# Kernel optimization log

Hardware: AMD Instinct MI355X
Metric: run time of the kernel (lower is better)

## Reference

```python
import jax, jax.numpy as jnp
import numpy as np

NUM_CATEGORIES = 32
INPUT_DIM = 1024
HIDDEN_DIM = 4096
BATCH = 64
SEQ = 512


def setup_inputs() -> dict:
    key = jax.random.key(0)
    k_x, k_w, k_c = jax.random.split(key, 3)
    x = jax.random.normal(k_x, (BATCH, SEQ, INPUT_DIM), dtype=jnp.float32)
    W = 0.02 * jax.random.normal(k_w, (NUM_CATEGORIES, INPUT_DIM, HIDDEN_DIM), dtype=jnp.float32)
    b = jnp.zeros((NUM_CATEGORIES, HIDDEN_DIM), dtype=jnp.float32)
    cat_ids = jax.random.randint(k_c, (BATCH,), 0, NUM_CATEGORIES, dtype=jnp.int64)
    return {"x": x, "cat_ids": cat_ids, "W": W, "b": b}


def reference(x, cat_ids, W, b):
    # Gather per-sample weight/bias by category, then batched matmul.
    selected_W = W[cat_ids]              # [B, input_dim, hidden_dim]
    selected_b = b[cat_ids]              # [B, hidden_dim]
    out = jnp.einsum('bsi,bih->bsh', x, selected_W)  # [B, S, hidden_dim]
    return out + selected_b[:, None, :]
```

## Files before the change

kernel.cpp:

```cpp
#include <hip/hip_runtime.h>
#include <stdint.h>

#define B_ 64
#define S_ 512
#define K_ 1024
#define H_ 4096
#define C_ 32

typedef float  f32x4  __attribute__((ext_vector_type(4)));
typedef short  bf16x8 __attribute__((ext_vector_type(8)));
typedef unsigned short u16x8 __attribute__((ext_vector_type(8)));
typedef __attribute__((address_space(3))) unsigned int as3u32;
typedef const __attribute__((address_space(1))) unsigned int as1u32;

__device__ __forceinline__ unsigned short f2bf(float f) {
    unsigned u = __builtin_bit_cast(unsigned, f);
    u += 0x7fffu + ((u >> 16) & 1u);
    return (unsigned short)(u >> 16);
}

__global__ void fix_cat_kernel(const void* __restrict__ cat_raw, int* __restrict__ cat32) {
    int t = threadIdx.x;
    const long long* c64 = (const long long*)cat_raw;
    const int*       c32 = (const int*)cat_raw;
    long long v = (t < 32) ? c64[t] : 0;
    int bad = (t < 32) && (v < 0 || v >= C_);
    unsigned long long m = __ballot(bad);
    if (m == 0ULL) {
        cat32[t] = (int)c64[t];
    } else {
        cat32[t] = c32[t];
    }
}

__global__ __launch_bounds__(256) void cvt_x_kernel(const float4* __restrict__ x,
                                                    uint4* __restrict__ xb, int n8) {
    int stride = gridDim.x * blockDim.x;
    for (int i = blockIdx.x * blockDim.x + threadIdx.x; i < n8; i += stride) {
        float4 a = x[2 * i], b = x[2 * i + 1];
        uint4 o;
        o.x = (unsigned)f2bf(a.x) | ((unsigned)f2bf(a.y) << 16);
        o.y = (unsigned)f2bf(a.z) | ((unsigned)f2bf(a.w) << 16);
        o.z = (unsigned)f2bf(b.x) | ((unsigned)f2bf(b.y) << 16);
        o.w = (unsigned)f2bf(b.z) | ((unsigned)f2bf(b.w) << 16);
        xb[i] = o;
    }
}

__global__ __launch_bounds__(256) void cvt_w_kernel(const float* __restrict__ W,
                                                    unsigned short* __restrict__ WT) {
    __shared__ unsigned short tile[64 * 68];
    const int nt = blockIdx.x;
    const int kt = blockIdx.y;
    const int c  = blockIdx.z;
    const int t  = threadIdx.x;

    const float* Wp = W + ((size_t)c << 22);
#pragma unroll
    for (int p = 0; p < 4; ++p) {
        int task = p * 256 + t;
        int kr = task >> 4;
        int nc = (task & 15) << 2;
        float4 v = *(const float4*)(Wp + (size_t)(kt * 64 + kr) * H_ + nt * 64 + nc);
        tile[kr * 68 + nc + 0] = f2bf(v.x);
        tile[kr * 68 + nc + 1] = f2bf(v.y);
        tile[kr * 68 + nc + 2] = f2bf(v.z);
        tile[kr * 68 + nc + 3] = f2bf(v.w);
    }
    __syncthreads();

    unsigned short* WTp = WT + ((size_t)c << 22);
#pragma unroll
    for (int q = 0; q < 2; ++q) {
        int task = q * 256 + t;
        int nl = task >> 3;
        int ko = (task & 7) << 3;
        u16x8 o;
#pragma unroll
        for (int j = 0; j < 8; ++j) o[j] = tile[(ko + j) * 68 + nl];
        *(u16x8*)(WTp + (size_t)(nt * 64 + nl) * K_ + kt * 64 + ko) = o;
    }
}

__global__ __launch_bounds__(512, 2) void gemm6_kernel(
    const unsigned short* __restrict__ xb,
    const unsigned short* __restrict__ WT,
    const float* __restrict__ bias,
    const int* __restrict__ cat,
    float* __restrict__ out)
{
    extern __shared__ __align__(16) char smem[];

    const int t    = threadIdx.x;
    const int lane = t & 63;
    const int w    = t >> 6;
    const int wm   = w >> 2;
    const int wn   = w & 3;
    const int lo   = lane & 15;
    const int hi   = lane >> 4;

    const int wg = (blockIdx.x & 7) * 256 + (blockIdx.x >> 3);
    const int bn = wg & 15;
    const int bm = (wg >> 4) & 1;
    const int bb = wg >> 5;

    const int c = cat[bb];

    const unsigned short* Ap = xb + (size_t)bb * (S_ * K_) + (size_t)(bm * 256) * K_;
    const unsigned short* Bp = WT + (size_t)c * ((size_t)H_ * K_) + (size_t)(bn * 256) * K_;

    const int srow  = lane >> 2;
    const int sslot = (lane & 3) ^ ((lane >> 3) & 3);
    const char* sA0 = (const char*)(Ap + (size_t)((0 * 8 + w) * 16 + srow) * K_) + sslot * 16;
    const char* sA1 = (const char*)(Ap + (size_t)((1 * 8 + w) * 16 + srow) * K_) + sslot * 16;
    const char* sB0 = (const char*)(Bp + (size_t)((0 * 8 + w) * 16 + srow) * K_) + sslot * 16;
    const char* sB1 = (const char*)(Bp + (size_t)((1 * 8 + w) * 16 + srow) * K_) + sslot * 16;
    const int dc0 = (0 * 8 + w) * 1024;
    const int dc1 = (1 * 8 + w) * 1024;

    const int xslot = (hi ^ ((lo >> 1) & 3)) << 4;
    int aoff[8], boff[4];
#pragma unroll
    for (int mi = 0; mi < 8; ++mi) aoff[mi] = (wm * 128 + mi * 16 + lo) * 64 + xslot;
#pragma unroll
    for (int ni = 0; ni < 4; ++ni) boff[ni] = 16384 + (wn * 64 + ni * 16 + lo) * 64 + xslot;

    f32x4 acc[8][4];
#pragma unroll
    for (int mi = 0; mi < 8; ++mi)
#pragma unroll
        for (int ni = 0; ni < 4; ++ni) acc[mi][ni] = f32x4{0.f, 0.f, 0.f, 0.f};

#define GLD(src_, dst_) __builtin_amdgcn_global_load_lds((as1u32*)(src_), (as3u32*)(dst_), 16, 0, 0)

    {
        char* s0 = smem;
        char* s1 = smem + 32768;
        GLD(sA0 + 0,  s0 + dc0);          GLD(sB0 + 0,  s0 + 16384 + dc0);
        GLD(sA1 + 0,  s0 + dc1);          GLD(sB1 + 0,  s0 + 16384 + dc1);
        GLD(sA0 + 64, s1 + dc0);          GLD(sB0 + 64, s1 + 16384 + dc0);
        GLD(sA1 + 64, s1 + dc1);          GLD(sB1 + 64, s1 + 16384 + dc1);
    }
    asm volatile("s_waitcnt vmcnt(4)" ::: "memory");
    __builtin_amdgcn_s_barrier();

    int rs = 0;
    int ws = 2;

#pragma unroll 1
    for (int T = 0; T < 32; ++T) {
        const char* rb = smem + rs * 32768;
        char*       wb = smem + ws * 32768;
        const int soff = ((T + 2) & 31) * 64;
        bf16x8 av[4], bv[4], aw[4];

#pragma unroll
        for (int mi = 0; mi < 4; ++mi) av[mi] = *(const bf16x8*)(rb + aoff[mi]);
#pragma unroll
        for (int ni = 0; ni < 4; ++ni) bv[ni] = *(const bf16x8*)(rb + boff[ni]);
        GLD(sA0 + soff, wb + dc0);
        GLD(sB0 + soff, wb + 16384 + dc0);
        __builtin_amdgcn_s_barrier();
        __builtin_amdgcn_s_setprio(1);
#pragma unroll
        for (int mi = 0; mi < 4; ++mi)
#pragma unroll
            for (int ni = 0; ni < 4; ++ni)
                acc[mi][ni] = __builtin_amdgcn_mfma_f32_16x16x32_bf16(
                    bv[ni], av[mi], acc[mi][ni], 0, 0, 0);
        __builtin_amdgcn_s_setprio(0);

#pragma unroll
        for (int mi = 0; mi < 4; ++mi) aw[mi] = *(const bf16x8*)(rb + aoff[mi + 4]);
        GLD(sA1 + soff, wb + dc1);
        GLD(sB1 + soff, wb + 16384 + dc1);
        asm volatile("s_waitcnt vmcnt(4)" ::: "memory");
        __builtin_amdgcn_s_barrier();
        __builtin_amdgcn_s_setprio(1);
#pragma unroll
        for (int mi = 0; mi < 4; ++mi)
#pragma unroll
            for (int ni = 0; ni < 4; ++ni)
                acc[mi + 4][ni] = __builtin_amdgcn_mfma_f32_16x16x32_bf16(
                    bv[ni], aw[mi], acc[mi + 4][ni], 0, 0, 0);
        __builtin_amdgcn_s_setprio(0);

        rs = (rs == 2) ? 0 : rs + 1;
        ws = (ws == 2) ? 0 : ws + 1;
    }
#undef GLD

    asm volatile("s_waitcnt vmcnt(0)" ::: "memory");

    float* outp = out + ((size_t)bb * S_ + bm * 256 + wm * 128) * H_ + bn * 256 + wn * 64;
    const float* bp = bias + (size_t)c * H_ + bn * 256 + wn * 64;
#pragma unroll
    for (int ni = 0; ni < 4; ++ni) {
        const int nf = ni * 16 + hi * 4;
        const f32x4 b4 = *(const f32x4*)(bp + nf);
#pragma unroll
        for (int mi = 0; mi < 8; ++mi) {
            const int mf = mi * 16 + lo;
            f32x4 v = acc[mi][ni];
            v.x += b4.x; v.y += b4.y; v.z += b4.z; v.w += b4.w;
            __builtin_nontemporal_store(v, (f32x4*)(outp + (size_t)mf * H_ + nf));
        }
    }
}

__global__ __launch_bounds__(256) void fallback_kernel(
    const float* __restrict__ x, const int* __restrict__ cat,
    const float* __restrict__ W, const float* __restrict__ bias,
    float* __restrict__ out)
{
    __shared__ float xs[K_];
    int bs = blockIdx.x;
    int bb = bs >> 9;
    int c  = cat[bb];
    const float* xp = x + (size_t)bs * K_;
    for (int i = threadIdx.x; i < K_ / 4; i += 256)
        ((float4*)xs)[i] = ((const float4*)xp)[i];
    __syncthreads();

    int h = blockIdx.y * 1024 + threadIdx.x * 4;
    const float* Wp = W + (size_t)c * K_ * H_ + h;
    float a0 = 0.f, a1 = 0.f, a2 = 0.f, a3 = 0.f;
    for (int k = 0; k < K_; ++k) {
        float xv = xs[k];
        float4 wv = *(const float4*)(Wp + (size_t)k * H_);
        a0 += xv * wv.x; a1 += xv * wv.y; a2 += xv * wv.z; a3 += xv * wv.w;
    }
    float4 bv = *(const float4*)(bias + c * H_ + h);
    float4 o; o.x = a0 + bv.x; o.y = a1 + bv.y; o.z = a2 + bv.z; o.w = a3 + bv.w;
    *(float4*)(out + (size_t)bs * H_ + h) = o;
}

extern "C" void kernel_launch(void* const* d_in, const int* in_sizes, int n_in,
                              void* d_out, int out_size, void* d_ws, size_t ws_size,
                              hipStream_t stream) {
    const float* x        = (const float*)d_in[0];
    const void*  cat_raw  = d_in[1];
    const float* W        = (const float*)d_in[2];
    const float* bias     = (const float*)d_in[3];
    float*       out      = (float*)d_out;

    const size_t CAT_BYTES = 256;
    const size_t XB_OFF    = 256;
    const size_t XB_BYTES  = (size_t)B_ * S_ * K_ * 2;
    const size_t WT_OFF    = XB_OFF + XB_BYTES;
    const size_t WT_BYTES  = (size_t)C_ * H_ * K_ * 2;
    const size_t NEED      = WT_OFF + WT_BYTES;

    const int* catp;
    if (ws_size >= CAT_BYTES) {
        int* cat32 = (int*)d_ws;
        fix_cat_kernel<<<1, 64, 0, stream>>>(cat_raw, cat32);
        catp = cat32;
    } else {
        catp = (const int*)cat_raw;
    }

    if (ws_size >= NEED) {
        unsigned short* xb = (unsigned short*)((char*)d_ws + XB_OFF);
        unsigned short* WT = (unsigned short*)((char*)d_ws + WT_OFF);
        cvt_x_kernel<<<2048, 256, 0, stream>>>((const float4*)x, (uint4*)xb,
                                               (int)((size_t)B_ * S_ * K_ / 8));
        dim3 gw(64, 16, 32);
        cvt_w_kernel<<<gw, 256, 0, stream>>>(W, WT);
        (void)hipFuncSetAttribute((const void*)gemm6_kernel,
                                  hipFuncAttributeMaxDynamicSharedMemorySize, 98304);
        gemm6_kernel<<<2048, 512, 98304, stream>>>(xb, WT, bias, catp, out);
    } else {
        dim3 g(B_ * S_, H_ / 1024);
        fallback_kernel<<<g, 256, 0, stream>>>(x, catp, W, bias, out);
    }
}
```

Measured before the change: 536.8 us.

## Halve GEMM M-tile to 128 rows and raise occupancy to four blocks per CU

The block tile shrinks from 256x256 to 128x256. Each wave now holds a 64x64 accumulator instead of 128x64, and the grid doubles to 4096 blocks. LDS per block drops to 72KB and launch bounds request 4 waves-per-EU occupancy, which lowers register pressure and should let more blocks overlap. The two-phase split of each K step and the setprio hints are removed. The cost is lower arithmetic intensity: the B tile is reloaded from memory for twice as many blocks, and there is a barrier per K step with less MFMA work between barriers.

```diff
diff --git a/kernel.cpp b/kernel.cpp
--- a/kernel.cpp
+++ b/kernel.cpp
@@ -82,7 +82,7 @@
     }
 }
 
-__global__ __launch_bounds__(512, 2) void gemm6_kernel(
+__global__ __launch_bounds__(512, 4) void gemm7_kernel(
     const unsigned short* __restrict__ xb,
     const unsigned short* __restrict__ WT,
     const float* __restrict__ bias,
@@ -99,35 +99,35 @@
     const int lo   = lane & 15;
     const int hi   = lane >> 4;
 
-    const int wg = (blockIdx.x & 7) * 256 + (blockIdx.x >> 3);
+    const int wg = (blockIdx.x & 7) * 512 + (blockIdx.x >> 3);
     const int bn = wg & 15;
-    const int bm = (wg >> 4) & 1;
-    const int bb = wg >> 5;
+    const int bm = (wg >> 4) & 3;
+    const int bb = wg >> 6;
 
     const int c = cat[bb];
 
-    const unsigned short* Ap = xb + (size_t)bb * (S_ * K_) + (size_t)(bm * 256) * K_;
+    const unsigned short* Ap = xb + (size_t)bb * (S_ * K_) + (size_t)(bm * 128) * K_;
     const unsigned short* Bp = WT + (size_t)c * ((size_t)H_ * K_) + (size_t)(bn * 256) * K_;
 
     const int srow  = lane >> 2;
     const int sslot = (lane & 3) ^ ((lane >> 3) & 3);
-    const char* sA0 = (const char*)(Ap + (size_t)((0 * 8 + w) * 16 + srow) * K_) + sslot * 16;
-    const char* sA1 = (const char*)(Ap + (size_t)((1 * 8 + w) * 16 + srow) * K_) + sslot * 16;
-    const char* sB0 = (const char*)(Bp + (size_t)((0 * 8 + w) * 16 + srow) * K_) + sslot * 16;
-    const char* sB1 = (const char*)(Bp + (size_t)((1 * 8 + w) * 16 + srow) * K_) + sslot * 16;
-    const int dc0 = (0 * 8 + w) * 1024;
-    const int dc1 = (1 * 8 + w) * 1024;
+    const char* sA0 = (const char*)(Ap + (size_t)(w * 16 + srow) * K_) + sslot * 16;
+    const char* sB0 = (const char*)(Bp + (size_t)(w * 16 + srow) * K_) + sslot * 16;
+    const char* sB1 = (const char*)(Bp + (size_t)((128 + w * 16) + srow) * K_) + sslot * 16;
+    const int dcA  = w * 1024;
+    const int dcB0 = 8192 + w * 1024;
+    const int dcB1 = 8192 + (8 + w) * 1024;
 
     const int xslot = (hi ^ ((lo >> 1) & 3)) << 4;
-    int aoff[8], boff[4];
-#pragma unroll
-    for (int mi = 0; mi < 8; ++mi) aoff[mi] = (wm * 128 + mi * 16 + lo) * 64 + xslot;
-#pragma unroll
-    for (int ni = 0; ni < 4; ++ni) boff[ni] = 16384 + (wn * 64 + ni * 16 + lo) * 64 + xslot;
-
-    f32x4 acc[8][4];
-#pragma unroll
-    for (int mi = 0; mi < 8; ++mi)
+    int aoff[4], boff[4];
+#pragma unroll
+    for (int mi = 0; mi < 4; ++mi) aoff[mi] = (wm * 64 + mi * 16 + lo) * 64 + xslot;
+#pragma unroll
+    for (int ni = 0; ni < 4; ++ni) boff[ni] = 8192 + (wn * 64 + ni * 16 + lo) * 64 + xslot;
+
+    f32x4 acc[4][4];
+#pragma unroll
+    for (int mi = 0; mi < 4; ++mi)
 #pragma unroll
         for (int ni = 0; ni < 4; ++ni) acc[mi][ni] = f32x4{0.f, 0.f, 0.f, 0.f};
 
@@ -135,13 +135,11 @@
 
     {
         char* s0 = smem;
-        char* s1 = smem + 32768;
-        GLD(sA0 + 0,  s0 + dc0);          GLD(sB0 + 0,  s0 + 16384 + dc0);
-        GLD(sA1 + 0,  s0 + dc1);          GLD(sB1 + 0,  s0 + 16384 + dc1);
-        GLD(sA0 + 64, s1 + dc0);          GLD(sB0 + 64, s1 + 16384 + dc0);
-        GLD(sA1 + 64, s1 + dc1);          GLD(sB1 + 64, s1 + 16384 + dc1);
-    }
-    asm volatile("s_waitcnt vmcnt(4)" ::: "memory");
+        char* s1 = smem + 24576;
+        GLD(sA0 + 0,  s0 + dcA); GLD(sB0 + 0,  s0 + dcB0); GLD(sB1 + 0,  s0 + dcB1);
+        GLD(sA0 + 64, s1 + dcA); GLD(sB0 + 64, s1 + dcB0); GLD(sB1 + 64, s1 + dcB1);
+    }
+    asm volatile("s_waitcnt vmcnt(3)" ::: "memory");
     __builtin_amdgcn_s_barrier();
 
     int rs = 0;
@@ -149,41 +147,27 @@
 
 #pragma unroll 1
     for (int T = 0; T < 32; ++T) {
-        const char* rb = smem + rs * 32768;
-        char*       wb = smem + ws * 32768;
+        const char* rb = smem + rs * 24576;
+        char*       wb = smem + ws * 24576;
         const int soff = ((T + 2) & 31) * 64;
-        bf16x8 av[4], bv[4], aw[4];
+        bf16x8 av[4], bv[4];
 
 #pragma unroll
         for (int mi = 0; mi < 4; ++mi) av[mi] = *(const bf16x8*)(rb + aoff[mi]);
 #pragma unroll
         for (int ni = 0; ni < 4; ++ni) bv[ni] = *(const bf16x8*)(rb + boff[ni]);
-        GLD(sA0 + soff, wb + dc0);
-        GLD(sB0 + soff, wb + 16384 + dc0);
+        GLD(sA0 + soff, wb + dcA);
+        GLD(sB0 + soff, wb + dcB0);
+        GLD(sB1 + soff, wb + dcB1);
+        asm volatile("s_waitcnt vmcnt(3)" ::: "memory");
         __builtin_amdgcn_s_barrier();
-        __builtin_amdgcn_s_setprio(1);
+
 #pragma unroll
         for (int mi = 0; mi < 4; ++mi)
 #pragma unroll
             for (int ni = 0; ni < 4; ++ni)
                 acc[mi][ni] = __builtin_amdgcn_mfma_f32_16x16x32_bf16(
                     bv[ni], av[mi], acc[mi][ni], 0, 0, 0);
-        __builtin_amdgcn_s_setprio(0);
-
-#pragma unroll
-        for (int mi = 0; mi < 4; ++mi) aw[mi] = *(const bf16x8*)(rb + aoff[mi + 4]);
-        GLD(sA1 + soff, wb + dc1);
-        GLD(sB1 + soff, wb + 16384 + dc1);
-        asm volatile("s_waitcnt vmcnt(4)" ::: "memory");
-        __builtin_amdgcn_s_barrier();
-        __builtin_amdgcn_s_setprio(1);
-#pragma unroll
-        for (int mi = 0; mi < 4; ++mi)
-#pragma unroll
-            for (int ni = 0; ni < 4; ++ni)
-                acc[mi + 4][ni] = __builtin_amdgcn_mfma_f32_16x16x32_bf16(
-                    bv[ni], aw[mi], acc[mi + 4][ni], 0, 0, 0);
-        __builtin_amdgcn_s_setprio(0);
 
         rs = (rs == 2) ? 0 : rs + 1;
         ws = (ws == 2) ? 0 : ws + 1;
@@ -192,14 +176,14 @@
 
     asm volatile("s_waitcnt vmcnt(0)" ::: "memory");
 
-    float* outp = out + ((size_t)bb * S_ + bm * 256 + wm * 128) * H_ + bn * 256 + wn * 64;
+    float* outp = out + ((size_t)bb * S_ + bm * 128 + wm * 64) * H_ + bn * 256 + wn * 64;
     const float* bp = bias + (size_t)c * H_ + bn * 256 + wn * 64;
 #pragma unroll
     for (int ni = 0; ni < 4; ++ni) {
         const int nf = ni * 16 + hi * 4;
         const f32x4 b4 = *(const f32x4*)(bp + nf);
 #pragma unroll
-        for (int mi = 0; mi < 8; ++mi) {
+        for (int mi = 0; mi < 4; ++mi) {
             const int mf = mi * 16 + lo;
             f32x4 v = acc[mi][ni];
             v.x += b4.x; v.y += b4.y; v.z += b4.z; v.w += b4.w;
@@ -267,9 +251,9 @@
                                                (int)((size_t)B_ * S_ * K_ / 8));
         dim3 gw(64, 16, 32);
         cvt_w_kernel<<<gw, 256, 0, stream>>>(W, WT);
-        (void)hipFuncSetAttribute((const void*)gemm6_kernel,
-                                  hipFuncAttributeMaxDynamicSharedMemorySize, 98304);
-        gemm6_kernel<<<2048, 512, 98304, stream>>>(xb, WT, bias, catp, out);
+        (void)hipFuncSetAttribute((const void*)gemm7_kernel,
+                                  hipFuncAttributeMaxDynamicSharedMemorySize, 73728);
+        gemm7_kernel<<<4096, 512, 73728, stream>>>(xb, WT, bias, catp, out);
     } else {
         dim3 g(B_ * S_, H_ / 1024);
         fallback_kernel<<<g, 256, 0, stream>>>(x, catp, W, bias, out);
```

Measured after the change: 596.6 us. 11.1% more time.

## Make GEMM persistent with cross-tile prefetch of next tile's first K slices

Applied to the files above, without the earlier changes.

The GEMM launch drops from 2048 workgroups to 256 persistent workgroups, each looping over 8 output tiles. During the last two K iterations of one tile it issues the loads for the next tile's first two K slices, so the pipeline prologue and drain overlap with compute. The epilogue stores run inside the loop and the accumulators are reset after each tile. The cost is fewer workgroups (256 of 512 threads with launch bounds for 2 per CU), which may underfill the 256-CU device's occupancy, plus extra address decoding and select logic in the hot loop.

```diff
diff --git a/kernel.cpp b/kernel.cpp
--- a/kernel.cpp
+++ b/kernel.cpp
@@ -82,7 +82,7 @@
     }
 }
 
-__global__ __launch_bounds__(512, 2) void gemm6_kernel(
+__global__ __launch_bounds__(512, 2) void gemm8_kernel(
     const unsigned short* __restrict__ xb,
     const unsigned short* __restrict__ WT,
     const float* __restrict__ bias,
@@ -99,22 +99,13 @@
     const int lo   = lane & 15;
     const int hi   = lane >> 4;
 
-    const int wg = (blockIdx.x & 7) * 256 + (blockIdx.x >> 3);
-    const int bn = wg & 15;
-    const int bm = (wg >> 4) & 1;
-    const int bb = wg >> 5;
-
-    const int c = cat[bb];
-
-    const unsigned short* Ap = xb + (size_t)bb * (S_ * K_) + (size_t)(bm * 256) * K_;
-    const unsigned short* Bp = WT + (size_t)c * ((size_t)H_ * K_) + (size_t)(bn * 256) * K_;
+    const int p = blockIdx.x;
 
     const int srow  = lane >> 2;
     const int sslot = (lane & 3) ^ ((lane >> 3) & 3);
-    const char* sA0 = (const char*)(Ap + (size_t)((0 * 8 + w) * 16 + srow) * K_) + sslot * 16;
-    const char* sA1 = (const char*)(Ap + (size_t)((1 * 8 + w) * 16 + srow) * K_) + sslot * 16;
-    const char* sB0 = (const char*)(Bp + (size_t)((0 * 8 + w) * 16 + srow) * K_) + sslot * 16;
-    const char* sB1 = (const char*)(Bp + (size_t)((1 * 8 + w) * 16 + srow) * K_) + sslot * 16;
+    const size_t re0 = (size_t)((0 * 8 + w) * 16 + srow) * K_;
+    const size_t re1 = (size_t)((1 * 8 + w) * 16 + srow) * K_;
+    const int sb  = sslot * 16;
     const int dc0 = (0 * 8 + w) * 1024;
     const int dc1 = (1 * 8 + w) * 1024;
 
@@ -131,15 +122,32 @@
 #pragma unroll
         for (int ni = 0; ni < 4; ++ni) acc[mi][ni] = f32x4{0.f, 0.f, 0.f, 0.f};
 
+#define DECODE(r_, A0_, A1_, B0_, B1_, bn_, bm_, bb_, c_) do {                     \
+    int aa__ = (r_) * 256 + p;                                                     \
+    int wg__ = (aa__ & 7) * 256 + (aa__ >> 3);                                     \
+    bn_ = wg__ & 15; bm_ = (wg__ >> 4) & 1; bb_ = wg__ >> 5;                       \
+    c_ = cat[bb_];                                                                 \
+    const unsigned short* Ap__ = xb + (size_t)bb_ * (S_ * K_) + (size_t)(bm_ * 256) * K_; \
+    const unsigned short* Bp__ = WT + (size_t)c_ * ((size_t)H_ * K_) + (size_t)(bn_ * 256) * K_; \
+    A0_ = (const char*)(Ap__ + re0) + sb; A1_ = (const char*)(Ap__ + re1) + sb;    \
+    B0_ = (const char*)(Bp__ + re0) + sb; B1_ = (const char*)(Bp__ + re1) + sb;    \
+} while (0)
+
 #define GLD(src_, dst_) __builtin_amdgcn_global_load_lds((as1u32*)(src_), (as3u32*)(dst_), 16, 0, 0)
+
+    const char *cA0, *cA1, *cB0, *cB1;
+    const char *nA0, *nA1, *nB0, *nB1;
+    int bn, bm, bb, cc, nbn, nbm, nbb, ncc;
+
+    DECODE(0, cA0, cA1, cB0, cB1, bn, bm, bb, cc);
 
     {
         char* s0 = smem;
         char* s1 = smem + 32768;
-        GLD(sA0 + 0,  s0 + dc0);          GLD(sB0 + 0,  s0 + 16384 + dc0);
-        GLD(sA1 + 0,  s0 + dc1);          GLD(sB1 + 0,  s0 + 16384 + dc1);
-        GLD(sA0 + 64, s1 + dc0);          GLD(sB0 + 64, s1 + 16384 + dc0);
-        GLD(sA1 + 64, s1 + dc1);          GLD(sB1 + 64, s1 + 16384 + dc1);
+        GLD(cA0 + 0,  s0 + dc0);          GLD(cB0 + 0,  s0 + 16384 + dc0);
+        GLD(cA1 + 0,  s0 + dc1);          GLD(cB1 + 0,  s0 + 16384 + dc1);
+        GLD(cA0 + 64, s1 + dc0);          GLD(cB0 + 64, s1 + 16384 + dc0);
+        GLD(cA1 + 64, s1 + dc1);          GLD(cB1 + 64, s1 + 16384 + dc1);
     }
     asm volatile("s_waitcnt vmcnt(4)" ::: "memory");
     __builtin_amdgcn_s_barrier();
@@ -147,65 +155,83 @@
     int rs = 0;
     int ws = 2;
 
+    for (int r = 0; r < 8; ++r) {
+        const int rn = (r < 7) ? (r + 1) : 7;
+        DECODE(rn, nA0, nA1, nB0, nB1, nbn, nbm, nbb, ncc);
+
 #pragma unroll 1
-    for (int T = 0; T < 32; ++T) {
-        const char* rb = smem + rs * 32768;
-        char*       wb = smem + ws * 32768;
-        const int soff = ((T + 2) & 31) * 64;
-        bf16x8 av[4], bv[4], aw[4];
-
-#pragma unroll
-        for (int mi = 0; mi < 4; ++mi) av[mi] = *(const bf16x8*)(rb + aoff[mi]);
-#pragma unroll
-        for (int ni = 0; ni < 4; ++ni) bv[ni] = *(const bf16x8*)(rb + boff[ni]);
-        GLD(sA0 + soff, wb + dc0);
-        GLD(sB0 + soff, wb + 16384 + dc0);
-        __builtin_amdgcn_s_barrier();
-        __builtin_amdgcn_s_setprio(1);
-#pragma unroll
-        for (int mi = 0; mi < 4; ++mi)
-#pragma unroll
-            for (int ni = 0; ni < 4; ++ni)
-                acc[mi][ni] = __builtin_amdgcn_mfma_f32_16x16x32_bf16(
-                    bv[ni], av[mi], acc[mi][ni], 0, 0, 0);
-        __builtin_amdgcn_s_setprio(0);
-
-#pragma unroll
-        for (int mi = 0; mi < 4; ++mi) aw[mi] = *(const bf16x8*)(rb + aoff[mi + 4]);
-        GLD(sA1 + soff, wb + dc1);
-        GLD(sB1 + soff, wb + 16384 + dc1);
-        asm volatile("s_waitcnt vmcnt(4)" ::: "memory");
-        __builtin_amdgcn_s_barrier();
-        __builtin_amdgcn_s_setprio(1);
-#pragma unroll
-        for (int mi = 0; mi < 4; ++mi)
-#pragma unroll
-            for (int ni = 0; ni < 4; ++ni)
-                acc[mi + 4][ni] = __builtin_amdgcn_mfma_f32_16x16x32_bf16(
-                    bv[ni], aw[mi], acc[mi + 4][ni], 0, 0, 0);
-        __builtin_amdgcn_s_setprio(0);
-
-        rs = (rs == 2) ? 0 : rs + 1;
-        ws = (ws == 2) ? 0 : ws + 1;
+        for (int T = 0; T < 32; ++T) {
+            const char* rb = smem + rs * 32768;
+            char*       wb = smem + ws * 32768;
+            const bool  nx = (T >= 30);
+            const char* pA0 = nx ? nA0 : cA0;
+            const char* pA1 = nx ? nA1 : cA1;
+            const char* pB0 = nx ? nB0 : cB0;
+            const char* pB1 = nx ? nB1 : cB1;
+            const int soff = ((T + 2) & 31) * 64;
+            bf16x8 av[4], bv[4], aw[4];
+
+#pragma unroll
+            for (int mi = 0; mi < 4; ++mi) av[mi] = *(const bf16x8*)(rb + aoff[mi]);
+#pragma unroll
+            for (int ni = 0; ni < 4; ++ni) bv[ni] = *(const bf16x8*)(rb + boff[ni]);
+            GLD(pA0 + soff, wb + dc0);
+            GLD(pB0 + soff, wb + 16384 + dc0);
+            __builtin_amdgcn_s_barrier();
+            __builtin_amdgcn_s_setprio(1);
+#pragma unroll
+            for (int mi = 0; mi < 4; ++mi)
+#pragma unroll
+                for (int ni = 0; ni < 4; ++ni)
+                    acc[mi][ni] = __builtin_amdgcn_mfma_f32_16x16x32_bf16(
+                        bv[ni], av[mi], acc[mi][ni], 0, 0, 0);
+            __builtin_amdgcn_s_setprio(0);
+
+#pragma unroll
+            for (int mi = 0; mi < 4; ++mi) aw[mi] = *(const bf16x8*)(rb + aoff[mi + 4]);
+            GLD(pA1 + soff, wb + dc1);
+            GLD(pB1 + soff, wb + 16384 + dc1);
+            asm volatile("s_waitcnt vmcnt(4)" ::: "memory");
+            __builtin_amdgcn_s_barrier();
+            __builtin_amdgcn_s_setprio(1);
+#pragma unroll
+            for (int mi = 0; mi < 4; ++mi)
+#pragma unroll
+                for (int ni = 0; ni < 4; ++ni)
+                    acc[mi + 4][ni] = __builtin_amdgcn_mfma_f32_16x16x32_bf16(
+                        bv[ni], aw[mi], acc[mi + 4][ni], 0, 0, 0);
+            __builtin_amdgcn_s_setprio(0);
+
+            rs = (rs == 2) ? 0 : rs + 1;
+            ws = (ws == 2) ? 0 : ws + 1;
+        }
+
+        {
+            float* outp = out + ((size_t)bb * S_ + bm * 256 + wm * 128) * H_
+                        + bn * 256 + wn * 64;
+            const float* bp = bias + (size_t)cc * H_ + bn * 256 + wn * 64;
+#pragma unroll
+            for (int ni = 0; ni < 4; ++ni) {
+                const int nf = ni * 16 + hi * 4;
+                const f32x4 b4 = *(const f32x4*)(bp + nf);
+#pragma unroll
+                for (int mi = 0; mi < 8; ++mi) {
+                    const int mf = mi * 16 + lo;
+                    f32x4 v = acc[mi][ni];
+                    v.x += b4.x; v.y += b4.y; v.z += b4.z; v.w += b4.w;
+                    __builtin_nontemporal_store(v, (f32x4*)(outp + (size_t)mf * H_ + nf));
+                    acc[mi][ni] = f32x4{0.f, 0.f, 0.f, 0.f};
+                }
+            }
+        }
+
+        cA0 = nA0; cA1 = nA1; cB0 = nB0; cB1 = nB1;
+        bn = nbn; bm = nbm; bb = nbb; cc = ncc;
     }
 #undef GLD
+#undef DECODE
 
     asm volatile("s_waitcnt vmcnt(0)" ::: "memory");
-
-    float* outp = out + ((size_t)bb * S_ + bm * 256 + wm * 128) * H_ + bn * 256 + wn * 64;
-    const float* bp = bias + (size_t)c * H_ + bn * 256 + wn * 64;
-#pragma unroll
-    for (int ni = 0; ni < 4; ++ni) {
-        const int nf = ni * 16 + hi * 4;
-        const f32x4 b4 = *(const f32x4*)(bp + nf);
-#pragma unroll
-        for (int mi = 0; mi < 8; ++mi) {
-            const int mf = mi * 16 + lo;
-            f32x4 v = acc[mi][ni];
-            v.x += b4.x; v.y += b4.y; v.z += b4.z; v.w += b4.w;
-            __builtin_nontemporal_store(v, (f32x4*)(outp + (size_t)mf * H_ + nf));
-        }
-    }
 }
 
 __global__ __launch_bounds__(256) void fallback_kernel(
@@ -267,9 +293,9 @@
                                                (int)((size_t)B_ * S_ * K_ / 8));
         dim3 gw(64, 16, 32);
         cvt_w_kernel<<<gw, 256, 0, stream>>>(W, WT);
-        (void)hipFuncSetAttribute((const void*)gemm6_kernel,
+        (void)hipFuncSetAttribute((const void*)gemm8_kernel,
                                   hipFuncAttributeMaxDynamicSharedMemorySize, 98304);
-        gemm6_kernel<<<2048, 512, 98304, stream>>>(xb, WT, bias, catp, out);
+        gemm8_kernel<<<256, 512, 98304, stream>>>(xb, WT, bias, catp, out);
     } else {
         dim3 g(B_ * S_, H_ / 1024);
         fallback_kernel<<<g, 256, 0, stream>>>(x, catp, W, bias, out);
```

Result: no change. 536.0 us (median of 3 runs) (-0.2%).
